# Performance work log

Hardware: AMD Instinct MI355X
Metric: run time of the kernel (lower is better)

## Reference

```python
import jax, jax.numpy as jnp
import numpy as np

N = 512      # hidden_size
L = 16384    # sequence length


def _make_hippo_legs(n_dim):
    # make_HiPPO_legs from the source
    b = jnp.sqrt(1.0 + 2.0 * jnp.arange(n_dim, dtype=jnp.float32))
    a = b[:, None] * b[None, :]
    a = jnp.tril(a) - jnp.diag(jnp.arange(n_dim, dtype=jnp.float32))
    return -a, b


def setup_inputs() -> dict:
    key = jax.random.key(0)
    c_key, x_key = jax.random.split(key, 2)
    A, Bv = _make_hippo_legs(N)
    B = Bv[:, None]                                   # (N, 1)
    C = jax.random.normal(c_key, (1, N), dtype=jnp.float32)
    in_x = jax.random.normal(x_key, (L,), dtype=jnp.float32)
    hidden_state = jnp.zeros((N,), dtype=jnp.float32)
    return {"in_x": in_x, "hidden_state": hidden_state, "A": A, "B": B, "C": C}


def reference(in_x, hidden_state, A, B, C):
    # discretize (bilinear / Tustin) with step = 1/L
    step = 1.0 / in_x.shape[0]
    I = jnp.eye(A.shape[0], dtype=A.dtype)
    BL = jnp.linalg.inv(I - (step / 2.0) * A)
    Ab = BL @ (I + (step / 2.0) * A)                  # (N, N)
    Bb = (BL * step) @ B                              # (N, 1)

    def step_through_time(h, x):
        # x: (1,) ; h: (N,)
        h_new = Ab @ h + Bb @ x                       # (N,)
        return h_new, C @ h_new                      # output (1,)

    new_hidden_state, output = jax.lax.scan(step_through_time, hidden_state, in_x[:, None])
    return output.squeeze(), new_hidden_state
```

## Files before the change

### kernel.cpp

```cpp
#include <hip/hip_runtime.h>

#define NDIM 512
#define LSEQ 16384
#define TCH  1024
#define PCH  16
#define MM   (NDIM * NDIM)

#define DTF  (1.0f/16384.0f)
#define DT2F (0.5f/16384.0f)

__device__ __forceinline__ void gkt(float* smem,
    const float* A, int lda, const float* B, int ldb,
    float* D, int ldd, int row0, int col0, int K, float alpha,
    float* Abe = nullptr, float* Bbce = nullptr, float* Ve = nullptr,
    const float* Bve = nullptr, int gr0 = -1, int gc0 = 0)
{
    const int tid  = threadIdx.x;
    const int w    = tid >> 6;
    const int lane = tid & 63;
    const int ty = lane >> 3, tx = lane & 7;

    float* As = smem + w * 1152;
    float* Bs = As + 576;

    const int Kc    = K >> 2;
    const int steps = Kc >> 4;
    const int kbase = w * Kc;

    const int ar  = lane >> 2, acg = (lane & 3) * 4;
    const int bkr = lane >> 3, bcg = (lane & 7) * 4;
    const float* Ap0 = A + (size_t)(row0 + ar) * lda + kbase + acg;
    const float* Ap1 = Ap0 + (size_t)16 * lda;
    const float* Bp0 = B + (size_t)(kbase + bkr) * ldb + col0 + bcg;
    const float* Bp1 = Bp0 + (size_t)8 * ldb;

    float4 av0 = *(const float4*)Ap0;
    float4 av1 = *(const float4*)Ap1;
    float4 bv0 = *(const float4*)Bp0;
    float4 bv1 = *(const float4*)Bp1;

    float acc[4][4] = {};

    for (int s = 0; s < steps; ++s) {
        As[(acg + 0) * 36 + ar] = av0.x;
        As[(acg + 1) * 36 + ar] = av0.y;
        As[(acg + 2) * 36 + ar] = av0.z;
        As[(acg + 3) * 36 + ar] = av0.w;
        As[(acg + 0) * 36 + ar + 16] = av1.x;
        As[(acg + 1) * 36 + ar + 16] = av1.y;
        As[(acg + 2) * 36 + ar + 16] = av1.z;
        As[(acg + 3) * 36 + ar + 16] = av1.w;
        *(float4*)(Bs + bkr * 36 + bcg)       = bv0;
        *(float4*)(Bs + (bkr + 8) * 36 + bcg) = bv1;

        if (s + 1 < steps) {
            int ko = (s + 1) * 16;
            av0 = *(const float4*)(Ap0 + ko);
            av1 = *(const float4*)(Ap1 + ko);
            bv0 = *(const float4*)(Bp0 + (size_t)ko * ldb);
            bv1 = *(const float4*)(Bp1 + (size_t)ko * ldb);
        }

#pragma unroll
        for (int kk = 0; kk < 16; ++kk) {
            float4 a = *(const float4*)(As + kk * 36 + 4 * ty);
            float4 b = *(const float4*)(Bs + kk * 36 + 4 * tx);
            acc[0][0] += a.x * b.x; acc[0][1] += a.x * b.y; acc[0][2] += a.x * b.z; acc[0][3] += a.x * b.w;
            acc[1][0] += a.y * b.x; acc[1][1] += a.y * b.y; acc[1][2] += a.y * b.z; acc[1][3] += a.y * b.w;
            acc[2][0] += a.z * b.x; acc[2][1] += a.z * b.y; acc[2][2] += a.z * b.z; acc[2][3] += a.z * b.w;
            acc[3][0] += a.w * b.x; acc[3][1] += a.w * b.y; acc[3][2] += a.w * b.z; acc[3][3] += a.w * b.w;
        }
    }

    float* red = smem + w * 1152;
#pragma unroll
    for (int i = 0; i < 4; ++i)
        *(float4*)(red + (4 * ty + i) * 32 + 4 * tx) =
            make_float4(acc[i][0], acc[i][1], acc[i][2], acc[i][3]);
    __syncthreads();

    float4 s0 = *(const float4*)(smem + 0 * 1152 + tid * 4);
    float4 s1 = *(const float4*)(smem + 1 * 1152 + tid * 4);
    float4 s2 = *(const float4*)(smem + 2 * 1152 + tid * 4);
    float4 s3 = *(const float4*)(smem + 3 * 1152 + tid * 4);
    float4 r4 = make_float4(alpha * (s0.x + s1.x + s2.x + s3.x),
                            alpha * (s0.y + s1.y + s2.y + s3.y),
                            alpha * (s0.z + s1.z + s2.z + s3.z),
                            alpha * (s0.w + s1.w + s2.w + s3.w));
    int r = tid >> 3, c = (tid & 7) * 4;
    float* dp = D + (size_t)(row0 + r) * ldd + col0 + c;
    dp[0] = r4.x; dp[1] = r4.y; dp[2] = r4.z; dp[3] = r4.w;

    if (gr0 >= 0) {
        int grow = gr0 + row0 + r, gcol = gc0 + col0 + c;
        *(float4*)(Abe + (size_t)grow * NDIM + gcol) =
            make_float4(2.f * r4.x, 2.f * r4.y, 2.f * r4.z, 2.f * r4.w);
        float pv = r4.x * Bve[gcol]     + r4.y * Bve[gcol + 1]
                 + r4.z * Bve[gcol + 2] + r4.w * Bve[gcol + 3];
        pv += __shfl_xor(pv, 1, 64);
        pv += __shfl_xor(pv, 2, 64);
        pv += __shfl_xor(pv, 4, 64);
        if ((tid & 7) == 0) {
            float bb = DTF * pv;
            atomicAdd(&Bbce[grow], bb);
            atomicAdd(&Ve[(size_t)grow * TCH], bb);
        }
    }
}

__device__ __forceinline__ void tri_decode(int t, int& it, int& jt)
{
    it = (int)((sqrtf(8.f * (float)t + 1.f) - 1.f) * 0.5f);
    while ((it + 1) * (it + 2) / 2 <= t) ++it;
    while (it * (it + 1) / 2 > t) --it;
    jt = t - it * (it + 1) / 2;
}

__device__ __forceinline__ void scan_task(int task, const float* G,
    const float* Zold, float* Znew, const float* hs, float* Hmat,
    float* hfin, int o, int last)
{
    int wid = task * 4 + (threadIdx.x >> 6);
    int lane = threadIdx.x & 63;
    int p = wid & (PCH - 1), i = wid >> 4;
    float dot = 0.f;
    if (p >= o) {
        const float* gr = G + (size_t)i * NDIM;
        const float* zc = Zold + (size_t)(p - o) * NDIM;
        int rmax = i >> 6;
        for (int r = 0; r <= rmax; ++r) {
            int k = (r << 6) + lane;
            if (k <= i) dot += gr[k] * zc[k];
        }
#pragma unroll
        for (int off = 32; off; off >>= 1) dot += __shfl_xor(dot, off, 64);
    }
    if (lane == 0) {
        float z = Zold[(size_t)p * NDIM + i] + dot;
        Znew[(size_t)p * NDIM + i] = z;
        if (last) {
            if (p < PCH - 1) Hmat[(size_t)(p + 1) * NDIM + i] = z;
            else hfin[i] = z;
            if (p == 0) Hmat[i] = hs[i];
        }
    }
}

__global__ __launch_bounds__(256) void zero_diag(const float* __restrict__ A,
    float* __restrict__ W, float* __restrict__ P0, float* __restrict__ Ab,
    float* __restrict__ Bbc, float* __restrict__ V, float* __restrict__ Crows,
    const float* __restrict__ Bv, const float* __restrict__ C)
{
    __shared__ float sh[64][65];
    __shared__ float sh2[64][65];
    const int t = blockIdx.x, tid = threadIdx.x;
    if (t < 8) {
        const int base = t * 64;
        for (int idx = tid; idx < 4096; idx += 256) {
            int r = idx >> 6, c = idx & 63;
            sh[r][c] = ((r == c) ? 1.f : 0.f)
                     - DT2F * A[(size_t)(base + r) * NDIM + base + c];
        }
        __syncthreads();
        if (tid < 64) {
            const int lane = tid;
            float xcol[64];
#pragma unroll
            for (int i = 0; i < 64; ++i) {
                float dot = 0.f;
#pragma unroll
                for (int k = 0; k < i; ++k) dot += sh[i][k] * xcol[k];
                xcol[i] = (((lane == i) ? 1.f : 0.f) - dot) / sh[i][i];
            }
#pragma unroll
            for (int k = 0; k < 64; ++k) {
                W[(size_t)(base + k) * NDIM + base + lane] = xcol[k];
                sh2[k][lane] = xcol[k];
            }
        }
        __syncthreads();
        for (int idx = tid; idx < 4096; idx += 256) {
            int r = idx >> 6, c = idx & 63;
            Ab[(size_t)(base + r) * NDIM + base + c] =
                2.f * sh2[r][c] - ((r == c) ? 1.f : 0.f);
        }
        {
            int k = tid >> 2, q = tid & 3;
            const float* xr = &sh2[k][0];
            float pv = 0.f;
#pragma unroll
            for (int c = 0; c < 16; ++c)
                pv += xr[q * 16 + c] * Bv[base + q * 16 + c];
            pv += __shfl_xor(pv, 1, 64);
            pv += __shfl_xor(pv, 2, 64);
            if (q == 0) {
                float bb = DTF * pv;
                Bbc[base + k] = bb;
                V[(size_t)(base + k) * TCH] = bb;
            }
        }
    } else if (t < 56) {
        const int q = (t - 8) >> 3, d = (t - 8) & 7;
        float* buf = P0 + (size_t)q * MM;
        for (int idx = tid; idx < 4096; idx += 256) {
            int r = idx >> 6, c = idx & 63;
            if (c > r) buf[(size_t)(d * 64 + r) * NDIM + d * 64 + c] = 0.f;
        }
    } else {
        Crows[tid]       = C[tid];
        Crows[tid + 256] = C[tid + 256];
    }
}

__global__ __launch_bounds__(256) void pair64(const float* __restrict__ A,
    float* __restrict__ W, float* __restrict__ T, float* __restrict__ Ab,
    float* __restrict__ Bbc, float* __restrict__ V, const float* __restrict__ Bv)
{
    __shared__ float smem[4608];
    const int o = blockIdx.x * 128;
#pragma unroll
    for (int t = 0; t < 4; ++t) {
        int it = t >> 1, jt = t & 1;
        gkt(smem, A + (size_t)(o + 64) * NDIM + o, NDIM,
            W + (size_t)o * NDIM + o, NDIM,
            T + (size_t)(o + 64) * NDIM + o, NDIM,
            it * 32, jt * 32, 64, 1.f);
        __syncthreads();
    }
#pragma unroll
    for (int t = 0; t < 4; ++t) {
        int it = t >> 1, jt = t & 1;
        gkt(smem, W + (size_t)(o + 64) * NDIM + (o + 64), NDIM,
            T + (size_t)(o + 64) * NDIM + o, NDIM,
            W + (size_t)(o + 64) * NDIM + o, NDIM,
            it * 32, jt * 32, 64, DT2F, Ab, Bbc, V, Bv, o + 64, o);
        __syncthreads();
    }
}

__global__ __launch_bounds__(256) void pairA2(const float* __restrict__ A,
    const float* __restrict__ W, float* __restrict__ T, int s)
{
    __shared__ float smem[4608];
    int ntx = s >> 5;
    int tile = blockIdx.x;
    int it = tile / ntx, jt = tile - it * ntx;
    int o = blockIdx.y * 2 * s;
    int col0 = jt * 32, k0 = col0 & ~63;
    gkt(smem, A + (size_t)(o + s) * NDIM + o + k0, NDIM,
        W + (size_t)(o + k0) * NDIM + o, NDIM,
        T + (size_t)(o + s) * NDIM + o, NDIM,
        it * 32, col0, s - k0, 1.f);
}

__global__ __launch_bounds__(256) void pairB2(float* __restrict__ W,
    const float* __restrict__ T, int s, float* __restrict__ Ab,
    float* __restrict__ Bbc, float* __restrict__ V, const float* __restrict__ Bv)
{
    __shared__ float smem[4608];
    int ntx = s >> 5;
    int tile = blockIdx.x;
    int it = tile / ntx, jt = tile - it * ntx;
    int o = blockIdx.y * 2 * s;
    int ke = (it * 32 + 95) & ~63; if (ke > s) ke = s;
    gkt(smem, W + (size_t)(o + s) * NDIM + (o + s), NDIM,
        T + (size_t)(o + s) * NDIM + o, NDIM,
        W + (size_t)(o + s) * NDIM + o, NDIM,
        it * 32, jt * 32, ke, DT2F, Ab, Bbc, V, Bv, o + s, o);
}

__global__ __launch_bounds__(256) void round_kernel(
    const float* __restrict__ g, float* __restrict__ gnew,
    float* __restrict__ V, float* __restrict__ Crows,
    int m, int lognx, int nz, int tailmode,
    const float* __restrict__ Gscan, const float* __restrict__ Ab,
    const float* __restrict__ x, const float* __restrict__ hs,
    const float* __restrict__ Bbc, float* __restrict__ kv,
    float* __restrict__ U, const float* __restrict__ Zin,
    float* __restrict__ Zout, float* __restrict__ Hmat,
    float* __restrict__ hfin, int o)
{
    __shared__ float smem[4608];
    const int t = blockIdx.x;
    const int tid = threadIdx.x;
    const int wv = tid >> 6, lane = tid & 63;

    if (t < 136) {
        int it, jt;
        tri_decode(t, it, jt);
        int k0 = (jt * 32) & ~63;
        int ke = (it * 32 + 95) & ~63; if (ke > NDIM) ke = NDIM;
        gkt(smem, g + k0, NDIM, g + (size_t)k0 * NDIM, NDIM,
            gnew, NDIM, it * 32, jt * 32, ke - k0, 1.f);
        return;
    }
    int u = t - 136;
    if (tailmode == 0) {
        int nmx = (m >= 32) ? (m >> 5) : 1;
        if (u < nz) {
            int it = u >> lognx, jt = u & (nmx - 1);
            int ke = (it * 32 + 95) & ~63; if (ke > NDIM) ke = NDIM;
            gkt(smem, g, NDIM, V, TCH, V + m, TCH, it * 32, jt * 32, ke, 1.f);
        } else {
            u -= nz;
            int it = u >> 4, jt = u & 15;
            int col0 = jt * 32, k0 = col0 & ~63;
            gkt(smem, Crows + k0, NDIM, g + (size_t)k0 * NDIM, NDIM,
                Crows + (size_t)m * NDIM, NDIM, it * 32, col0, NDIM - k0, 1.f);
        }
    } else if (tailmode == 1) {
        if (u < 2) {
            float* cs = smem;
            for (int k = tid; k < NDIM; k += 256)
                cs[k] = Crows[(size_t)1023 * NDIM + k];
            __syncthreads();
            int j = u * 256 + tid;
            int k0 = j & ~63;
            float acc = 0.f;
            for (int k = k0; k < NDIM; k += 4) {
                acc += cs[k]     * Ab[(size_t)k * NDIM + j]
                     + cs[k + 1] * Ab[(size_t)(k + 1) * NDIM + j]
                     + cs[k + 2] * Ab[(size_t)(k + 2) * NDIM + j]
                     + cs[k + 3] * Ab[(size_t)(k + 3) * NDIM + j];
            }
            Crows[(size_t)1024 * NDIM + j] = acc;
        } else if (u < 258) {
            int j = (u - 2) * 4 + wv;
            const float* cr = Crows + (size_t)j * NDIM;
            float dot = 0.f;
#pragma unroll
            for (int rr = 0; rr < 2; ++rr) {
                int oo = rr * 256 + lane * 4;
                float4 c4 = *(const float4*)(cr + oo);
                float4 b4 = *(const float4*)(Bbc + oo);
                dot += c4.x * b4.x + c4.y * b4.y + c4.z * b4.z + c4.w * b4.w;
            }
#pragma unroll
            for (int off = 32; off; off >>= 1) dot += __shfl_xor(dot, off, 64);
            if (lane == 0) kv[j] = dot;
        } else {
            int wid = (u - 258) * 4 + wv;
            int p = wid & (PCH - 1), i = wid >> 4;
            const float* vr = V + (size_t)i * TCH;
            const float* xc = x + p * TCH;
            float s = 0.f;
#pragma unroll
            for (int rr = 0; rr < 16; ++rr) {
                int t2 = (rr << 6) + lane;
                s += vr[TCH - 1 - t2] * xc[t2];
            }
            if (p == 0) {
                const float* gr = Gscan + (size_t)i * NDIM;
                int rmax = i >> 6;
                for (int rr = 0; rr <= rmax; ++rr) {
                    int k = (rr << 6) + lane;
                    if (k <= i) s += gr[k] * hs[k];
                }
            }
#pragma unroll
            for (int off = 32; off; off >>= 1) s += __shfl_xor(s, off, 64);
            if (lane == 0) U[(size_t)p * NDIM + i] = s;
        }
    } else {
        scan_task(u, Gscan, Zin, Zout, hs, Hmat, hfin, o, 0);
    }
}

__global__ __launch_bounds__(256) void scan_round(const float* __restrict__ G,
    const float* __restrict__ Zold, float* __restrict__ Znew,
    const float* __restrict__ hs, float* __restrict__ Hmat,
    float* __restrict__ hfin, int o, int last)
{
    scan_task(blockIdx.x, G, Zold, Znew, hs, Hmat, hfin, o, last);
}

__global__ __launch_bounds__(256) void emit(const float* __restrict__ Crows,
    const float* __restrict__ Hmat, const float* __restrict__ kv,
    const float* __restrict__ x, float* __restrict__ out)
{
    int wid = blockIdx.x * 4 + (threadIdx.x >> 6);
    int lane = threadIdx.x & 63;
    int p = wid & (PCH - 1), s = wid >> 4;
    const float* cr = Crows + (size_t)(s + 1) * NDIM;
    const float* hp = Hmat + (size_t)p * NDIM;
    float dot = 0.f;
#pragma unroll
    for (int r = 0; r < 2; ++r) {
        int o = r * 256 + lane * 4;
        float4 c = *(const float4*)(cr + o);
        float4 h = *(const float4*)(hp + o);
        dot += c.x * h.x + c.y * h.y + c.z * h.z + c.w * h.w;
    }
    const float* xc = x + p * TCH;
    int rmax = s >> 6;
    for (int r = 0; r <= rmax; ++r) {
        int t = (r << 6) + lane;
        if (t <= s) dot += kv[s - t] * xc[t];
    }
#pragma unroll
    for (int off = 32; off; off >>= 1) dot += __shfl_xor(dot, off, 64);
    if (lane == 0) out[p * TCH + s] = dot;
}

extern "C" void kernel_launch(void* const* d_in, const int* in_sizes, int n_in,
                              void* d_out, int out_size, void* d_ws, size_t ws_size,
                              hipStream_t stream)
{
    (void)in_sizes; (void)n_in; (void)out_size; (void)ws_size;
    const float* x  = (const float*)d_in[0];
    const float* hs = (const float*)d_in[1];
    const float* A  = (const float*)d_in[2];
    const float* Bv = (const float*)d_in[3];
    const float* C  = (const float*)d_in[4];
    float* out = (float*)d_out;

    float* ws     = (float*)d_ws;
    float* Ab     = ws;
    float* P0     = Ab + MM;
    float* P1     = P0 + MM;
    float* GA     = P1 + MM;
    float* GB     = GA + MM;
    float* GC     = GB + MM;
    float* GD     = GC + MM;
    float* V      = GD + MM;
    float* Crows  = V + NDIM * TCH;
    float* CrowsW = Crows + TCH * NDIM;
    float* kv     = CrowsW + TCH * NDIM;
    float* Bbc    = kv + TCH;
    float* U      = Bbc + NDIM;
    float* Z0     = U + PCH * NDIM;
    float* Z1     = Z0 + PCH * NDIM;
    float* Hmat   = Z1 + PCH * NDIM;

    float* W = CrowsW;
    float* T = P0;

    zero_diag<<<57, 256, 0, stream>>>(A, W, P0, Ab, Bbc, V, Crows, Bv, C);

    pair64<<<4, 256, 0, stream>>>(A, W, T, Ab, Bbc, V, Bv);
    for (int s = 128; s <= 256; s <<= 1) {
        int np = NDIM / (2 * s);
        int tiles = (s >> 5) * (s >> 5);
        dim3 grid(tiles, np);
        pairA2<<<grid, 256, 0, stream>>>(A, W, T, s);
        pairB2<<<grid, 256, 0, stream>>>(W, T, s, Ab, Bbc, V, Bv);
    }

    const float* g = Ab;
    float* gouts[13] = {P0, P1, P0, P1, P0, P1, P0, P1, P0, GA, GB, GC, GD};
    int m = 1;
    for (int r = 0; r < 13; ++r) {
        int nmx = (m >= 32) ? (m >> 5) : 1;
        int lognx = (r >= 5) ? (r - 5) : 0;
        int nz = (m < TCH) ? 16 * nmx : 0;
        int tailmode = 0, ntail = 0, oo = 0;
        const float* Gs = GA; const float* Zi = U; float* Zo = Z0;
        if (r == 10)      { tailmode = 1; ntail = 2306; }
        else if (r == 11) { tailmode = 2; ntail = 2048; oo = 1; }
        else if (r == 12) { tailmode = 2; ntail = 2048; oo = 2; Gs = GB;
                            Zi = Z0; Zo = Z1; }
        round_kernel<<<136 + 2 * nz + ntail, 256, 0, stream>>>(
            g, gouts[r], V, Crows, m, lognx, nz, tailmode, Gs, Ab,
            x, hs, Bbc, kv, U, Zi, Zo, Hmat, out + LSEQ, oo);
        g = gouts[r];
        m <<= 1;
    }

    scan_round<<<2048, 256, 0, stream>>>(GC, Z1, Z0, hs, Hmat, out + LSEQ, 4, 0);
    scan_round<<<2048, 256, 0, stream>>>(GD, Z0, Z1, hs, Hmat, out + LSEQ, 8, 1);

    emit<<<4096, 256, 0, stream>>>(Crows, Hmat, kv, x, out);
}
```

Baseline: 266.4 us.

## Fuse s=128 pair stage and final two scan rounds into single kernels

Replaces the pairA2/pairB2 launches at s=128 with a single pair128 kernel that does both phases per column tile, and merges the two final scan_round launches into one scan_final kernel of 16 blocks that computes both prefix-combination steps using shared memory. This cuts kernel launch count and the global round-trip of intermediate Z vectors between launches. The fused scan uses only 16 blocks doing triangular matvecs serially per wave, so parallelism drops sharply compared with 2048 blocks, which could make it a longer critical path.

```diff
diff --git a/kernel.cpp b/kernel.cpp
--- a/kernel.cpp
+++ b/kernel.cpp
@@ -234,6 +234,33 @@
             T + (size_t)(o + 64) * NDIM + o, NDIM,
             W + (size_t)(o + 64) * NDIM + o, NDIM,
             it * 32, jt * 32, 64, DT2F, Ab, Bbc, V, Bv, o + 64, o);
+        __syncthreads();
+    }
+}
+
+__global__ __launch_bounds__(256) void pair128(const float* __restrict__ A,
+    float* __restrict__ W, float* __restrict__ T, float* __restrict__ Ab,
+    float* __restrict__ Bbc, float* __restrict__ V, const float* __restrict__ Bv)
+{
+    __shared__ float smem[4608];
+    const int o   = (blockIdx.x >> 2) * 256;
+    const int jt  = blockIdx.x & 3;
+    const int col0 = jt * 32, k0 = col0 & ~63;
+#pragma unroll
+    for (int it = 0; it < 4; ++it) {
+        gkt(smem, A + (size_t)(o + 128) * NDIM + o + k0, NDIM,
+            W + (size_t)(o + k0) * NDIM + o, NDIM,
+            T + (size_t)(o + 128) * NDIM + o, NDIM,
+            it * 32, col0, 128 - k0, 1.f);
+        __syncthreads();
+    }
+#pragma unroll
+    for (int it = 0; it < 4; ++it) {
+        int ke = (it * 32 + 95) & ~63; if (ke > 128) ke = 128;
+        gkt(smem, W + (size_t)(o + 128) * NDIM + (o + 128), NDIM,
+            T + (size_t)(o + 128) * NDIM + o, NDIM,
+            W + (size_t)(o + 128) * NDIM + o, NDIM,
+            it * 32, col0, ke, DT2F, Ab, Bbc, V, Bv, o + 128, o);
         __syncthreads();
     }
 }
@@ -366,12 +393,66 @@
     }
 }
 
-__global__ __launch_bounds__(256) void scan_round(const float* __restrict__ G,
-    const float* __restrict__ Zold, float* __restrict__ Znew,
+__global__ __launch_bounds__(256) void scan_final(const float* __restrict__ GC,
+    const float* __restrict__ GD, const float* __restrict__ Z2,
     const float* __restrict__ hs, float* __restrict__ Hmat,
-    float* __restrict__ hfin, int o, int last)
-{
-    scan_task(blockIdx.x, G, Zold, Znew, hs, Hmat, hfin, o, last);
+    float* __restrict__ hfin)
+{
+    __shared__ float sv[NDIM];
+    __shared__ float sw[NDIM];
+    const int p = blockIdx.x;
+    const int tid = threadIdx.x;
+    const int wave = tid >> 6, lane = tid & 63;
+
+    const float* z4  = (p >= 4)  ? Z2 + (size_t)(p - 4)  * NDIM : nullptr;
+    const float* z8  = (p >= 8)  ? Z2 + (size_t)(p - 8)  * NDIM : nullptr;
+    const float* z12 = (p >= 12) ? Z2 + (size_t)(p - 12) * NDIM : nullptr;
+
+    for (int i = wave; i < NDIM; i += 4) {
+        float dv = 0.f, dw = 0.f;
+        if (p >= 4) {
+            const float* gr = GC + (size_t)i * NDIM;
+            int rmax = i >> 6;
+            for (int r = 0; r <= rmax; ++r) {
+                int k = (r << 6) + lane;
+                if (k <= i) {
+                    float gg = gr[k];
+                    if (z12) dv += gg * z12[k];
+                    dw += gg * z4[k];
+                }
+            }
+#pragma unroll
+            for (int off = 32; off; off >>= 1) {
+                dv += __shfl_xor(dv, off, 64);
+                dw += __shfl_xor(dw, off, 64);
+            }
+        }
+        if (lane == 0) {
+            sv[i] = (z8 ? z8[i] : 0.f) + dv;
+            sw[i] = dw;
+        }
+    }
+    __syncthreads();
+    for (int i = wave; i < NDIM; i += 4) {
+        float d = 0.f;
+        if (p >= 8) {
+            const float* gr = GD + (size_t)i * NDIM;
+            int rmax = i >> 6;
+            for (int r = 0; r <= rmax; ++r) {
+                int k = (r << 6) + lane;
+                if (k <= i) d += gr[k] * sv[k];
+            }
+#pragma unroll
+            for (int off = 32; off; off >>= 1) d += __shfl_xor(d, off, 64);
+        }
+        if (lane == 0) {
+            float z = Z2[(size_t)p * NDIM + i] + sw[i] + d;
+            if (p < PCH - 1) Hmat[(size_t)(p + 1) * NDIM + i] = z;
+            else hfin[i] = z;
+        }
+    }
+    if (p == 0)
+        for (int i = tid; i < NDIM; i += 256) Hmat[i] = hs[i];
 }
 
 __global__ __launch_bounds__(256) void emit(const float* __restrict__ Crows,
@@ -438,13 +519,9 @@
     zero_diag<<<57, 256, 0, stream>>>(A, W, P0, Ab, Bbc, V, Crows, Bv, C);
 
     pair64<<<4, 256, 0, stream>>>(A, W, T, Ab, Bbc, V, Bv);
-    for (int s = 128; s <= 256; s <<= 1) {
-        int np = NDIM / (2 * s);
-        int tiles = (s >> 5) * (s >> 5);
-        dim3 grid(tiles, np);
-        pairA2<<<grid, 256, 0, stream>>>(A, W, T, s);
-        pairB2<<<grid, 256, 0, stream>>>(W, T, s, Ab, Bbc, V, Bv);
-    }
+    pair128<<<8, 256, 0, stream>>>(A, W, T, Ab, Bbc, V, Bv);
+    pairA2<<<64, 256, 0, stream>>>(A, W, T, 256);
+    pairB2<<<64, 256, 0, stream>>>(W, T, 256, Ab, Bbc, V, Bv);
 
     const float* g = Ab;
     float* gouts[13] = {P0, P1, P0, P1, P0, P1, P0, P1, P0, GA, GB, GC, GD};
@@ -466,8 +543,7 @@
         m <<= 1;
     }
 
-    scan_round<<<2048, 256, 0, stream>>>(GC, Z1, Z0, hs, Hmat, out + LSEQ, 4, 0);
-    scan_round<<<2048, 256, 0, stream>>>(GD, Z0, Z1, hs, Hmat, out + LSEQ, 8, 1);
+    scan_final<<<PCH, 256, 0, stream>>>(GC, GD, Z1, hs, Hmat, out + LSEQ);
 
     emit<<<4096, 256, 0, stream>>>(Crows, Hmat, kv, x, out);
 }
```

After: 645.6 us. 142% more time.
